# Kernel optimization log

Measured on AMD Instinct MI355X. Metric: run time of the kernel, lower is better.

## Reference

```python
import jax, jax.numpy as jnp
import numpy as np

B, N, D, H, E, W, OUT = 4, 2048, 128, 4, 32768, 8, 128


def setup_inputs() -> dict:
    key = jax.random.key(0)
    ks = jax.random.split(key, 11)
    s = 0.05  # weight init scale
    return {
        "nodefeatures": jax.random.normal(ks[0], (B, N, D), jnp.float32),
        "node_indices": jax.random.randint(ks[1], (B, 2, E), 0, N),
        "nodeattributes": jax.random.uniform(ks[2], (B, E, W), jnp.float32),
        "wq_w": jax.random.normal(ks[3], (H, D, D), jnp.float32) * s,
        "wq_b": jax.random.normal(ks[4], (H, D), jnp.float32) * s,
        "wk_w": jax.random.normal(ks[5], (H, D, D), jnp.float32) * s,
        "wk_b": jax.random.normal(ks[6], (H, D), jnp.float32) * s,
        "wv_w": jax.random.normal(ks[7], (H, D, D), jnp.float32) * s,
        "wv_b": jax.random.normal(ks[8], (H, D), jnp.float32) * s,
        "out_w": jax.random.normal(ks[9], (OUT, H * D), jnp.float32) * s,
        "out_b": jax.random.normal(ks[10], (OUT,), jnp.float32) * s,
    }


def reference(nodefeatures, node_indices, nodeattributes,
              wq_w, wq_b, wk_w, wk_b, wv_w, wv_b, out_w, out_b):
    b, n, d = nodefeatures.shape
    h = wq_w.shape[0]
    # per-head Linear projections: y = x @ W.T + bias, batched over heads -> [b,h,n,d]
    q = jnp.einsum('bnd,hed->bhne', nodefeatures, wq_w) + wq_b[None, :, None, :]
    k = jnp.einsum('bnd,hed->bhne', nodefeatures, wk_w) + wk_b[None, :, None, :]
    v = jnp.einsum('bnd,hed->bhne', nodefeatures, wv_w) + wv_b[None, :, None, :]

    i = node_indices[:, 0, :]  # [b,E] row indices
    j = node_indices[:, 1, :]  # [b,E] col indices

    # gather q_i, k_j per edge -> [b,h,E,d]; edge score = <q_i,k_j>/sqrt(n)
    qi = jnp.take_along_axis(q, i[:, None, :, None], axis=2)
    kj = jnp.take_along_axis(k, j[:, None, :, None], axis=2)
    wsum = nodeattributes.sum(axis=-1)  # [b,E] (x_edge[:,None]*weights).sum(1)
    # original divides by k.shape[1]**0.5 == sqrt(n)
    edge = (qi * kj).sum(-1) / (n ** 0.5) * wsum[:, None, :]  # [b,h,E]

    # scatter edge scores into zero-initialized dense logits [b,h,n,n]
    bi = jnp.arange(b)[:, None, None]
    hi = jnp.arange(h)[None, :, None]
    scores = jnp.zeros((b, h, n, n), q.dtype).at[bi, hi, i[:, None, :], j[:, None, :]].set(edge)

    attn = jax.nn.softmax(scores, axis=-1)
    o = jnp.einsum('bhnm,bhmd->bhnd', attn, v)
    o = o.transpose(0, 2, 1, 3).reshape(b, n, h * d)  # concat heads on feature dim
    return o @ out_w.T + out_b
```

## Files before the change

### kernel.cpp

```cpp
#include <hip/hip_runtime.h>
#include <hip/hip_bf16.h>
#include <math.h>

constexpr int B_ = 4;
constexpr int N_ = 2048;
constexpr int D_ = 128;
constexpr int H_ = 4;
constexpr int E_ = 32768;
constexpr int W_ = 8;
constexpr int OUT_ = 128;
constexpr int HD_ = H_ * D_;
constexpr int C3_ = 3 * HD_;
constexpr int CAP = 64;
constexpr int M_ = B_ * N_;

typedef __attribute__((ext_vector_type(8))) __bf16 bf16x8;
typedef __attribute__((ext_vector_type(4))) float f32x4;
typedef unsigned int uint32;
typedef unsigned short u16;

__device__ __forceinline__ u16 f2b(float f) {
    __hip_bfloat16 h = __float2bfloat16(f);
    return *(u16*)&h;
}
__device__ __forceinline__ float blo(uint32 u) { return __uint_as_float(u << 16); }
__device__ __forceinline__ float bhi(uint32 u) { return __uint_as_float(u & 0xffff0000u); }

__device__ __forceinline__ void g2l16(const void* g, void* l) {
    __builtin_amdgcn_global_load_lds(
        (const __attribute__((address_space(1))) unsigned int*)(uintptr_t)g,
        (__attribute__((address_space(3))) unsigned int*)(uintptr_t)l,
        16, 0, 0);
}

__global__ __launch_bounds__(256) void prep_kernel(
    const float* __restrict__ X,
    const float* __restrict__ wq, const float* __restrict__ wk, const float* __restrict__ wv,
    const float* __restrict__ bq, const float* __restrict__ bk, const float* __restrict__ bv,
    const float* __restrict__ OW,
    u16* __restrict__ Xbf, u16* __restrict__ Wbf, float* __restrict__ biasf,
    u16* __restrict__ OWbf,
    int* __restrict__ row_count, float* __restrict__ vsum)
{
    const int blk = blockIdx.x;
    if (blk < 512) {
        const int tid = blk * 256 + threadIdx.x;
        const int row = tid >> 4, sub = tid & 15;
        const float4 f0 = *(const float4*)(X + (size_t)row * 128 + sub * 8);
        const float4 f1 = *(const float4*)(X + (size_t)row * 128 + sub * 8 + 4);
        union { u16 u[8]; uint4 v; } pk;
        pk.u[0]=f2b(f0.x); pk.u[1]=f2b(f0.y); pk.u[2]=f2b(f0.z); pk.u[3]=f2b(f0.w);
        pk.u[4]=f2b(f1.x); pk.u[5]=f2b(f1.y); pk.u[6]=f2b(f1.z); pk.u[7]=f2b(f1.w);
        const int ob = row * 256 + ((sub * 16) ^ ((row & 7) << 4));
        *(uint4*)((char*)Xbf + ob) = pk.v;
    } else if (blk < 608) {
        const int c = (blk - 512) * 256 + threadIdx.x;
        const int g = c >> 11, idx = c & 2047;
        const int t3 = g >> 2, h = g & 3;
        const float* Wsrc = (t3 == 0 ? wq : t3 == 1 ? wk : wv) + (size_t)h * 128 * 128;
        const int e = idx >> 4, sub = idx & 15;
        const float4 f0 = *(const float4*)(Wsrc + (size_t)e * 128 + sub * 8);
        const float4 f1 = *(const float4*)(Wsrc + (size_t)e * 128 + sub * 8 + 4);
        union { u16 u[8]; uint4 v; } pk;
        pk.u[0]=f2b(f0.x); pk.u[1]=f2b(f0.y); pk.u[2]=f2b(f0.z); pk.u[3]=f2b(f0.w);
        pk.u[4]=f2b(f1.x); pk.u[5]=f2b(f1.y); pk.u[6]=f2b(f1.z); pk.u[7]=f2b(f1.w);
        const int ob = g * 32768 + e * 256 + ((sub * 16) ^ ((e & 7) << 4));
        *(uint4*)((char*)Wbf + ob) = pk.v;
        if (idx < 128) {
            const float* Bsrc = (t3 == 0 ? bq : t3 == 1 ? bk : bv) + h * 128;
            biasf[g * 128 + idx] = Bsrc[idx];
        }
    } else if (blk < 640) {
        const int tid = (blk - 608) * 256 + threadIdx.x;
        const int c = tid >> 6, sub = tid & 63;
        const float4 f0 = *(const float4*)(OW + (size_t)c * 512 + sub * 8);
        const float4 f1 = *(const float4*)(OW + (size_t)c * 512 + sub * 8 + 4);
        union { u16 u[8]; uint4 v; } pk;
        pk.u[0]=f2b(f0.x); pk.u[1]=f2b(f0.y); pk.u[2]=f2b(f0.z); pk.u[3]=f2b(f0.w);
        pk.u[4]=f2b(f1.x); pk.u[5]=f2b(f1.y); pk.u[6]=f2b(f1.z); pk.u[7]=f2b(f1.w);
        const int ob = c * 1024 + ((sub * 16) ^ ((c & 7) << 4));
        *(uint4*)((char*)OWbf + ob) = pk.v;
    } else {
        const uint4 z = make_uint4(0, 0, 0, 0);
        uint4* rc = (uint4*)row_count;
        #pragma unroll
        for (int q = 0; q < 8; ++q) rc[threadIdx.x + q * 256] = z;
        uint4* vs = (uint4*)vsum;
        #pragma unroll
        for (int q = 0; q < 2; ++q) vs[threadIdx.x + q * 256] = z;
    }
}

__global__ __launch_bounds__(256) void append_kernel(
    const int* __restrict__ nidx, const float* __restrict__ attr,
    int* __restrict__ row_count, int2* __restrict__ row_edges)
{
    const int wave = threadIdx.x >> 6;
    const int lane = threadIdx.x & 63;
    const int gw = blockIdx.x * 4 + wave;
    const int e0g = gw * 8;
    const int b = e0g / E_;
    const int e0 = e0g % E_;

    float a = attr[((size_t)b * E_ + e0) * W_ + lane];
    a += __shfl_xor(a, 1);
    a += __shfl_xor(a, 2);
    a += __shfl_xor(a, 4);

    if ((lane & 7) == 0) {
        const int sub = lane >> 3;
        const int e = e0 + sub;
        const int i = nidx[b * 2 * E_ + e];
        const int j = nidx[b * 2 * E_ + E_ + e];
        const int pos = atomicAdd(&row_count[b * N_ + i], 1);
        if (pos < CAP)
            row_edges[(size_t)(b * N_ + i) * CAP + pos] =
                make_int2(e | (j << 16), __float_as_int(a));
    }
}

__global__ __launch_bounds__(256) void qkv_mfma(
    const u16* __restrict__ Xbf, const u16* __restrict__ Wbf,
    const float* __restrict__ biasf, u16* __restrict__ QKV,
    float* __restrict__ vsum)
{
    __shared__ u16 As[128 * 128];
    __shared__ u16 Bs[128 * 128];
    const int rb = blockIdx.x & 63;
    const int g  = blockIdx.x >> 6;
    const int t = threadIdx.x;
    const int lane = t & 63, wave = t >> 6;
    const int wm = wave >> 1, wn = wave & 1;
    const int l15 = lane & 15, l4 = lane >> 4;

    const char* Asrc = (const char*)(Xbf + (size_t)rb * 128 * 128);
    const char* Bsrc = (const char*)(Wbf + (size_t)g  * 128 * 128);
    #pragma unroll
    for (int q = 0; q < 8; ++q) {
        const int o = t * 16 + q * 4096;
        g2l16(Asrc + o, (char*)As + o);
        g2l16(Bsrc + o, (char*)Bs + o);
    }
    __syncthreads();

    f32x4 acc[4][4];
    #pragma unroll
    for (int i = 0; i < 4; ++i)
        #pragma unroll
        for (int j = 0; j < 4; ++j) acc[i][j] = (f32x4){0.f, 0.f, 0.f, 0.f};

    #pragma unroll
    for (int ks = 0; ks < 4; ++ks) {
        const int kb = ks * 64 + l4 * 16;
        bf16x8 a[4], bb[4];
        #pragma unroll
        for (int fm = 0; fm < 4; ++fm) {
            const int row = wm * 64 + fm * 16 + l15;
            a[fm] = *(const bf16x8*)((const char*)As + row * 256 + (kb ^ ((row & 7) << 4)));
        }
        #pragma unroll
        for (int fn = 0; fn < 4; ++fn) {
            const int col = wn * 64 + fn * 16 + l15;
            bb[fn] = *(const bf16x8*)((const char*)Bs + col * 256 + (kb ^ ((col & 7) << 4)));
        }
        #pragma unroll
        for (int fm = 0; fm < 4; ++fm)
            #pragma unroll
            for (int fn = 0; fn < 4; ++fn)
                acc[fm][fn] = __builtin_amdgcn_mfma_f32_16x16x32_bf16(
                    a[fm], bb[fn], acc[fm][fn], 0, 0, 0);
    }

    __syncthreads();

    #pragma unroll
    for (int fm = 0; fm < 4; ++fm)
        #pragma unroll
        for (int fn = 0; fn < 4; ++fn) {
            const int col = wn * 64 + fn * 16 + l15;
            const float bv = biasf[g * 128 + col];
            #pragma unroll
            for (int r = 0; r < 4; ++r) {
                const int row = wm * 64 + fm * 16 + l4 * 4 + r;
                *(u16*)((char*)As + row * 256 + ((col * 2) ^ ((row & 7) << 4))) =
                    f2b(acc[fm][fn][r] + bv);
            }
        }

    if (g >= 8) {
        const int h = g - 8;
        const int b = rb >> 4;
        #pragma unroll
        for (int fn = 0; fn < 4; ++fn) {
            float s = 0.f;
            #pragma unroll
            for (int fm = 0; fm < 4; ++fm)
                #pragma unroll
                for (int r = 0; r < 4; ++r) s += acc[fm][fn][r];
            s += __shfl_xor(s, 16);
            s += __shfl_xor(s, 32);
            if (l4 == 0) {
                const int col = wn * 64 + fn * 16 + l15;
                const float bv = biasf[g * 128 + col];
                atomicAdd(&vsum[(b * H_ + h) * 128 + col], s + 64.f * bv);
            }
        }
    }
    __syncthreads();

    #pragma unroll
    for (int q = 0; q < 8; ++q) {
        const int idx = t + q * 256;
        const int row = idx >> 4, c = idx & 15;
        const uint4 v = *(const uint4*)((char*)As + row * 256 + ((c * 16) ^ ((row & 7) << 4)));
        *(uint4*)(QKV + (size_t)(rb * 128 + row) * C3_ + g * 128 + c * 8) = v;
    }
}

__global__ __launch_bounds__(256) void row_fused(
    const u16* __restrict__ QKV, const float* __restrict__ vsum,
    const int* __restrict__ row_count, const int2* __restrict__ row_edges,
    u16* __restrict__ Obf)
{
    const int t = threadIdx.x;
    const int wave = t >> 6, lane = t & 63;
    const int row = blockIdx.x * 4 + wave;
    const int b = blockIdx.y;
    const int R = b * N_ + row;
    int cnt = row_count[R];
    if (cnt > CAP) cnt = CAP;

    int ej = 0; float ws = 0.f;
    if (lane < cnt) {
        const int2 v = row_edges[(size_t)R * CAP + lane];
        ej = v.x; ws = __int_as_float(v.y);
    }
    const int myj = ej >> 16, mye = ej & 0xFFFF;
    bool win = (lane < cnt);
    for (int p = 0; p < cnt; ++p) {
        const int oj = __shfl(ej, p);
        if (win && (oj >> 16) == myj && (oj & 0xFFFF) > mye) win = false;
    }
    unsigned long long m = __ballot(win);

    const char* base = (const char*)QKV;
    const uint4 qv = *(const uint4*)(base + (size_t)R * 3072 + lane * 16);
    const float q0=blo(qv.x), q1=bhi(qv.x), q2=blo(qv.y), q3=bhi(qv.y),
                q4=blo(qv.z), q5=bhi(qv.z), q6=blo(qv.w), q7=bhi(qv.w);
    const float rs = 0.02209708691207961f;

    float a0=0.f,a1=0.f,a2=0.f,a3=0.f,a4=0.f,a5=0.f,a6=0.f,a7=0.f;
    float dsum = 0.f;

#define PROCESS(kv, vv, wsp)                                                  \
    {                                                                         \
        float s = q0*blo(kv.x) + q1*bhi(kv.x) + q2*blo(kv.y) + q3*bhi(kv.y)   \
                + q4*blo(kv.z) + q5*bhi(kv.z) + q6*blo(kv.w) + q7*bhi(kv.w);  \
        s += __shfl_xor(s, 1);                                                \
        s += __shfl_xor(s, 2);                                                \
        s += __shfl_xor(s, 4);                                                \
        s += __shfl_xor(s, 8);                                                \
        const float x = expf(s * rs * (wsp)) - 1.f;                           \
        dsum += x;                                                            \
        a0 = fmaf(x, blo(vv.x), a0); a1 = fmaf(x, bhi(vv.x), a1);             \
        a2 = fmaf(x, blo(vv.y), a2); a3 = fmaf(x, bhi(vv.y), a3);             \
        a4 = fmaf(x, blo(vv.z), a4); a5 = fmaf(x, bhi(vv.z), a5);             \
        a6 = fmaf(x, blo(vv.w), a6); a7 = fmaf(x, bhi(vv.w), a7);             \
    }

    if (m) {
        int p = (int)__ffsll(m) - 1; m &= m - 1;
        int jc = __shfl(ej, p) >> 16;
        float wc = __shfl(ws, p);
        const char* nb = base + (size_t)(b * N_ + jc) * 3072;
        uint4 kv = *(const uint4*)(nb + 1024 + lane * 16);
        uint4 vv = *(const uint4*)(nb + 2048 + lane * 16);
        while (m) {
            const int p2 = (int)__ffsll(m) - 1; m &= m - 1;
            const int j2 = __shfl(ej, p2) >> 16;
            const float w2 = __shfl(ws, p2);
            const char* nb2 = base + (size_t)(b * N_ + j2) * 3072;
            const uint4 kv2 = *(const uint4*)(nb2 + 1024 + lane * 16);
            const uint4 vv2 = *(const uint4*)(nb2 + 2048 + lane * 16);
            PROCESS(kv, vv, wc);
            kv = kv2; vv = vv2; wc = w2;
        }
        PROCESS(kv, vv, wc);
    }
#undef PROCESS

    const float inv = 1.0f / (2048.0f + dsum);
    const float* vsp = vsum + (b * H_ + (lane >> 4)) * 128 + (lane & 15) * 8;
    const float4 vs0 = *(const float4*)vsp;
    const float4 vs1 = *(const float4*)(vsp + 4);
    union { u16 u[8]; uint4 v; } o;
    o.u[0]=f2b((vs0.x+a0)*inv); o.u[1]=f2b((vs0.y+a1)*inv);
    o.u[2]=f2b((vs0.z+a2)*inv); o.u[3]=f2b((vs0.w+a3)*inv);
    o.u[4]=f2b((vs1.x+a4)*inv); o.u[5]=f2b((vs1.y+a5)*inv);
    o.u[6]=f2b((vs1.z+a6)*inv); o.u[7]=f2b((vs1.w+a7)*inv);
    const int ob = ((lane >> 4) << 8) + (((lane & 15) * 16) ^ ((R & 7) << 4));
    *(uint4*)((char*)Obf + (size_t)R * 1024 + ob) = o.v;
}

__global__ __launch_bounds__(256) void out_mfma(
    const u16* __restrict__ Obf, const u16* __restrict__ OWbf,
    const float* __restrict__ bo, float* __restrict__ Out)
{
    __shared__ u16 As[64 * 128];
    __shared__ u16 Bs[128 * 128];
    const int rb = blockIdx.x;
    const int t = threadIdx.x;
    const int lane = t & 63, wave = t >> 6;
    const int wm = wave >> 1, wn = wave & 1;
    const int l15 = lane & 15, l4 = lane >> 4;

    f32x4 acc[2][4];
    #pragma unroll
    for (int i = 0; i < 2; ++i)
        #pragma unroll
        for (int j = 0; j < 4; ++j) acc[i][j] = (f32x4){0.f, 0.f, 0.f, 0.f};

    for (int kc = 0; kc < 4; ++kc) {
        #pragma unroll
        for (int q = 0; q < 4; ++q) {
            const int o = t * 16 + q * 4096;
            const int arow = o >> 8, ob = o & 255;
            g2l16((const char*)Obf + (size_t)(rb * 64 + arow) * 1024 + kc * 256 + ob,
                  (char*)As + o);
        }
        #pragma unroll
        for (int q = 0; q < 8; ++q) {
            const int o = t * 16 + q * 4096;
            const int c = o >> 8, ob = o & 255;
            g2l16((const char*)OWbf + (size_t)c * 1024 + kc * 256 + ob,
                  (char*)Bs + o);
        }
        __syncthreads();
        #pragma unroll
        for (int ks = 0; ks < 4; ++ks) {
            const int kb = ks * 64 + l4 * 16;
            bf16x8 a[2], bb[4];
            #pragma unroll
            for (int fm = 0; fm < 2; ++fm) {
                const int row = wm * 32 + fm * 16 + l15;
                a[fm] = *(const bf16x8*)((const char*)As + row * 256 + (kb ^ ((row & 7) << 4)));
            }
            #pragma unroll
            for (int fn = 0; fn < 4; ++fn) {
                const int col = wn * 64 + fn * 16 + l15;
                bb[fn] = *(const bf16x8*)((const char*)Bs + col * 256 + (kb ^ ((col & 7) << 4)));
            }
            #pragma unroll
            for (int fm = 0; fm < 2; ++fm)
                #pragma unroll
                for (int fn = 0; fn < 4; ++fn)
                    acc[fm][fn] = __builtin_amdgcn_mfma_f32_16x16x32_bf16(
                        a[fm], bb[fn], acc[fm][fn], 0, 0, 0);
        }
        __syncthreads();
    }

    #pragma unroll
    for (int fm = 0; fm < 2; ++fm)
        #pragma unroll
        for (int fn = 0; fn < 4; ++fn) {
            const int col = wn * 64 + fn * 16 + l15;
            const float bv = bo[col];
            #pragma unroll
            for (int r = 0; r < 4; ++r) {
                const int row = rb * 64 + wm * 32 + fm * 16 + l4 * 4 + r;
                Out[(size_t)row * OUT_ + col] = acc[fm][fn][r] + bv;
            }
        }
}

extern "C" void kernel_launch(void* const* d_in, const int* in_sizes, int n_in,
                              void* d_out, int out_size, void* d_ws, size_t ws_size,
                              hipStream_t stream)
{
    const float* x     = (const float*)d_in[0];
    const int*   nidx  = (const int*)  d_in[1];
    const float* attr  = (const float*)d_in[2];
    const float* wq_w  = (const float*)d_in[3];
    const float* wq_b  = (const float*)d_in[4];
    const float* wk_w  = (const float*)d_in[5];
    const float* wk_b  = (const float*)d_in[6];
    const float* wv_w  = (const float*)d_in[7];
    const float* wv_b  = (const float*)d_in[8];
    const float* out_w = (const float*)d_in[9];
    const float* out_b = (const float*)d_in[10];
    float* out = (float*)d_out;

    char* ws = (char*)d_ws;
    size_t off = 0;
    auto alloc = [&](size_t bytes) -> char* {
        char* p = ws + off;
        off += (bytes + 255) & ~(size_t)255;
        return p;
    };
    u16*  Xbf  = (u16*)alloc((size_t)M_ * D_ * 2);
    u16*  Wbf  = (u16*)alloc((size_t)12 * D_ * D_ * 2);
    float* biasf = (float*)alloc((size_t)12 * D_ * 4);
    u16*  QKV  = (u16*)alloc((size_t)M_ * C3_ * 2);
    u16*  OWbf = (u16*)alloc((size_t)OUT_ * HD_ * 2);
    u16*  Obf  = (u16*)alloc((size_t)M_ * HD_ * 2);
    float* vsum = (float*)alloc((size_t)B_ * H_ * D_ * 4);
    int*  row_count = (int*)alloc((size_t)B_ * N_ * 4);
    int2* row_edges = (int2*)alloc((size_t)B_ * N_ * CAP * 8);

    prep_kernel<<<641, 256, 0, stream>>>(
        x, wq_w, wk_w, wv_w, wq_b, wk_b, wv_b, out_w,
        Xbf, Wbf, biasf, OWbf, row_count, vsum);
    append_kernel<<<(B_ * E_) / 32, 256, 0, stream>>>(nidx, attr, row_count, row_edges);
    qkv_mfma<<<64 * 12, 256, 0, stream>>>(Xbf, Wbf, biasf, QKV, vsum);
    row_fused<<<dim3(N_ / 4, B_), 256, 0, stream>>>(
        QKV, vsum, row_count, row_edges, Obf);
    out_mfma<<<M_ / 64, 256, 0, stream>>>(Obf, OWbf, out_b, out);
}
```

Measured before the change: 84.24 us.

## Fuse edge append into QKV GEMM launch, double-buffer gathers, shrink output tiles

The edge-append pass now runs inside the QKV GEMM launch: 256 extra blocks, each looping 16 times, do the append alongside the 768 GEMM blocks. This removes one kernel launch and lets the append overlap the GEMM. The row kernel now fetches two neighbour K/V rows per step into two accumulator sets, which gives more memory-level parallelism. The output GEMM uses 32-row tiles, doubling the block count for better occupancy at the cost of reloading the weight tile more often. The appended blocks still allocate the GEMM's large shared memory, and the extra registers in the row kernel may lower its occupancy.

Result: faster. 79.18 us (-6.0%).

```diff
diff --git a/kernel.cpp b/kernel.cpp
--- a/kernel.cpp
+++ b/kernel.cpp
@@ -91,45 +91,45 @@
     }
 }
 
-__global__ __launch_bounds__(256) void append_kernel(
+__global__ __launch_bounds__(256) void qkv_append(
+    const u16* __restrict__ Xbf, const u16* __restrict__ Wbf,
+    const float* __restrict__ biasf,
     const int* __restrict__ nidx, const float* __restrict__ attr,
+    u16* __restrict__ QKV, float* __restrict__ vsum,
     int* __restrict__ row_count, int2* __restrict__ row_edges)
-{
-    const int wave = threadIdx.x >> 6;
-    const int lane = threadIdx.x & 63;
-    const int gw = blockIdx.x * 4 + wave;
-    const int e0g = gw * 8;
-    const int b = e0g / E_;
-    const int e0 = e0g % E_;
-
-    float a = attr[((size_t)b * E_ + e0) * W_ + lane];
-    a += __shfl_xor(a, 1);
-    a += __shfl_xor(a, 2);
-    a += __shfl_xor(a, 4);
-
-    if ((lane & 7) == 0) {
-        const int sub = lane >> 3;
-        const int e = e0 + sub;
-        const int i = nidx[b * 2 * E_ + e];
-        const int j = nidx[b * 2 * E_ + E_ + e];
-        const int pos = atomicAdd(&row_count[b * N_ + i], 1);
-        if (pos < CAP)
-            row_edges[(size_t)(b * N_ + i) * CAP + pos] =
-                make_int2(e | (j << 16), __float_as_int(a));
-    }
-}
-
-__global__ __launch_bounds__(256) void qkv_mfma(
-    const u16* __restrict__ Xbf, const u16* __restrict__ Wbf,
-    const float* __restrict__ biasf, u16* __restrict__ QKV,
-    float* __restrict__ vsum)
 {
     __shared__ u16 As[128 * 128];
     __shared__ u16 Bs[128 * 128];
+    const int t = threadIdx.x;
+    const int lane = t & 63, wave = t >> 6;
+
+    if (blockIdx.x >= 768) {
+        const int gw0 = (blockIdx.x - 768) * 4 + wave;
+        for (int it = 0; it < 16; ++it) {
+            const int gw = gw0 + it * 1024;
+            const int e0g = gw * 8;
+            const int b = e0g / E_;
+            const int e0 = e0g % E_;
+            float a = attr[((size_t)b * E_ + e0) * W_ + lane];
+            a += __shfl_xor(a, 1);
+            a += __shfl_xor(a, 2);
+            a += __shfl_xor(a, 4);
+            if ((lane & 7) == 0) {
+                const int sub = lane >> 3;
+                const int e = e0 + sub;
+                const int i = nidx[b * 2 * E_ + e];
+                const int j = nidx[b * 2 * E_ + E_ + e];
+                const int pos = atomicAdd(&row_count[b * N_ + i], 1);
+                if (pos < CAP)
+                    row_edges[(size_t)(b * N_ + i) * CAP + pos] =
+                        make_int2(e | (j << 16), __float_as_int(a));
+            }
+        }
+        return;
+    }
+
     const int rb = blockIdx.x & 63;
     const int g  = blockIdx.x >> 6;
-    const int t = threadIdx.x;
-    const int lane = t & 63, wave = t >> 6;
     const int wm = wave >> 1, wn = wave & 1;
     const int l15 = lane & 15, l4 = lane >> 4;
 
@@ -249,55 +249,65 @@
                 q4=blo(qv.z), q5=bhi(qv.z), q6=blo(qv.w), q7=bhi(qv.w);
     const float rs = 0.02209708691207961f;
 
-    float a0=0.f,a1=0.f,a2=0.f,a3=0.f,a4=0.f,a5=0.f,a6=0.f,a7=0.f;
-    float dsum = 0.f;
-
-#define PROCESS(kv, vv, wsp)                                                  \
-    {                                                                         \
-        float s = q0*blo(kv.x) + q1*bhi(kv.x) + q2*blo(kv.y) + q3*bhi(kv.y)   \
-                + q4*blo(kv.z) + q5*bhi(kv.z) + q6*blo(kv.w) + q7*bhi(kv.w);  \
-        s += __shfl_xor(s, 1);                                                \
-        s += __shfl_xor(s, 2);                                                \
-        s += __shfl_xor(s, 4);                                                \
-        s += __shfl_xor(s, 8);                                                \
-        const float x = expf(s * rs * (wsp)) - 1.f;                           \
-        dsum += x;                                                            \
-        a0 = fmaf(x, blo(vv.x), a0); a1 = fmaf(x, bhi(vv.x), a1);             \
-        a2 = fmaf(x, blo(vv.y), a2); a3 = fmaf(x, bhi(vv.y), a3);             \
-        a4 = fmaf(x, blo(vv.z), a4); a5 = fmaf(x, bhi(vv.z), a5);             \
-        a6 = fmaf(x, blo(vv.w), a6); a7 = fmaf(x, bhi(vv.w), a7);             \
-    }
+    float A0=0.f,A1=0.f,A2=0.f,A3=0.f,A4=0.f,A5=0.f,A6=0.f,A7=0.f;
+    float B0=0.f,B1=0.f,B2=0.f,B3=0.f,B4=0.f,B5=0.f,B6=0.f,B7=0.f;
+    float dsA = 0.f, dsB = 0.f;
+
+#define FETCH(MM, KV1,VV1,W1,KV2,VV2,W2,NN)                                  \
+    { int p_ = (int)__ffsll((long long)MM) - 1; MM &= MM - 1;                \
+      const int j_ = __shfl(ej, p_) >> 16; W1 = __shfl(ws, p_);              \
+      const char* nb_ = base + (size_t)(b * N_ + j_) * 3072;                 \
+      KV1 = *(const uint4*)(nb_ + 1024 + lane * 16);                         \
+      VV1 = *(const uint4*)(nb_ + 2048 + lane * 16);                         \
+      if (MM) {                                                              \
+        int q_ = (int)__ffsll((long long)MM) - 1; MM &= MM - 1;              \
+        const int j2_ = __shfl(ej, q_) >> 16; W2 = __shfl(ws, q_);           \
+        const char* nb2_ = base + (size_t)(b * N_ + j2_) * 3072;             \
+        KV2 = *(const uint4*)(nb2_ + 1024 + lane * 16);                      \
+        VV2 = *(const uint4*)(nb2_ + 2048 + lane * 16);                      \
+        NN = 2;                                                              \
+      } else NN = 1; }
+
+#define PROC(kv, vv, wsp, S)                                                 \
+    { float s_ = q0*blo(kv.x) + q1*bhi(kv.x) + q2*blo(kv.y) + q3*bhi(kv.y)   \
+               + q4*blo(kv.z) + q5*bhi(kv.z) + q6*blo(kv.w) + q7*bhi(kv.w);  \
+      s_ += __shfl_xor(s_, 1);                                               \
+      s_ += __shfl_xor(s_, 2);                                               \
+      s_ += __shfl_xor(s_, 4);                                               \
+      s_ += __shfl_xor(s_, 8);                                               \
+      const float x_ = expf(s_ * rs * (wsp)) - 1.f;                          \
+      ds##S += x_;                                                           \
+      S##0 = fmaf(x_, blo(vv.x), S##0); S##1 = fmaf(x_, bhi(vv.x), S##1);    \
+      S##2 = fmaf(x_, blo(vv.y), S##2); S##3 = fmaf(x_, bhi(vv.y), S##3);    \
+      S##4 = fmaf(x_, blo(vv.z), S##4); S##5 = fmaf(x_, bhi(vv.z), S##5);    \
+      S##6 = fmaf(x_, blo(vv.w), S##6); S##7 = fmaf(x_, bhi(vv.w), S##7); }
 
     if (m) {
-        int p = (int)__ffsll(m) - 1; m &= m - 1;
-        int jc = __shfl(ej, p) >> 16;
-        float wc = __shfl(ws, p);
-        const char* nb = base + (size_t)(b * N_ + jc) * 3072;
-        uint4 kv = *(const uint4*)(nb + 1024 + lane * 16);
-        uint4 vv = *(const uint4*)(nb + 2048 + lane * 16);
+        uint4 kv1, vv1, kv2, vv2; float w1, w2; int n1;
+        FETCH(m, kv1, vv1, w1, kv2, vv2, w2, n1);
         while (m) {
-            const int p2 = (int)__ffsll(m) - 1; m &= m - 1;
-            const int j2 = __shfl(ej, p2) >> 16;
-            const float w2 = __shfl(ws, p2);
-            const char* nb2 = base + (size_t)(b * N_ + j2) * 3072;
-            const uint4 kv2 = *(const uint4*)(nb2 + 1024 + lane * 16);
-            const uint4 vv2 = *(const uint4*)(nb2 + 2048 + lane * 16);
-            PROCESS(kv, vv, wc);
-            kv = kv2; vv = vv2; wc = w2;
-        }
-        PROCESS(kv, vv, wc);
-    }
-#undef PROCESS
-
-    const float inv = 1.0f / (2048.0f + dsum);
+            uint4 nk1, nv1, nk2, nv2; float nw1, nw2; int n2;
+            FETCH(m, nk1, nv1, nw1, nk2, nv2, nw2, n2);
+            PROC(kv1, vv1, w1, A);
+            if (n1 == 2) PROC(kv2, vv2, w2, B);
+            kv1 = nk1; vv1 = nv1; w1 = nw1;
+            kv2 = nk2; vv2 = nv2; w2 = nw2; n1 = n2;
+        }
+        PROC(kv1, vv1, w1, A);
+        if (n1 == 2) PROC(kv2, vv2, w2, B);
+    }
+#undef FETCH
+#undef PROC
+
+    const float inv = 1.0f / (2048.0f + dsA + dsB);
     const float* vsp = vsum + (b * H_ + (lane >> 4)) * 128 + (lane & 15) * 8;
     const float4 vs0 = *(const float4*)vsp;
     const float4 vs1 = *(const float4*)(vsp + 4);
     union { u16 u[8]; uint4 v; } o;
-    o.u[0]=f2b((vs0.x+a0)*inv); o.u[1]=f2b((vs0.y+a1)*inv);
-    o.u[2]=f2b((vs0.z+a2)*inv); o.u[3]=f2b((vs0.w+a3)*inv);
-    o.u[4]=f2b((vs1.x+a4)*inv); o.u[5]=f2b((vs1.y+a5)*inv);
-    o.u[6]=f2b((vs1.z+a6)*inv); o.u[7]=f2b((vs1.w+a7)*inv);
+    o.u[0]=f2b((vs0.x+A0+B0)*inv); o.u[1]=f2b((vs0.y+A1+B1)*inv);
+    o.u[2]=f2b((vs0.z+A2+B2)*inv); o.u[3]=f2b((vs0.w+A3+B3)*inv);
+    o.u[4]=f2b((vs1.x+A4+B4)*inv); o.u[5]=f2b((vs1.y+A5+B5)*inv);
+    o.u[6]=f2b((vs1.z+A6+B6)*inv); o.u[7]=f2b((vs1.w+A7+B7)*inv);
     const int ob = ((lane >> 4) << 8) + (((lane & 15) * 16) ^ ((R & 7) << 4));
     *(uint4*)((char*)Obf + (size_t)R * 1024 + ob) = o.v;
 }
@@ -306,7 +316,7 @@
     const u16* __restrict__ Obf, const u16* __restrict__ OWbf,
     const float* __restrict__ bo, float* __restrict__ Out)
 {
-    __shared__ u16 As[64 * 128];
+    __shared__ u16 As[32 * 128];
     __shared__ u16 Bs[128 * 128];
     const int rb = blockIdx.x;
     const int t = threadIdx.x;
@@ -314,18 +324,16 @@
     const int wm = wave >> 1, wn = wave & 1;
     const int l15 = lane & 15, l4 = lane >> 4;
 
-    f32x4 acc[2][4];
-    #pragma unroll
-    for (int i = 0; i < 2; ++i)
-        #pragma unroll
-        for (int j = 0; j < 4; ++j) acc[i][j] = (f32x4){0.f, 0.f, 0.f, 0.f};
+    f32x4 acc[4];
+    #pragma unroll
+    for (int j = 0; j < 4; ++j) acc[j] = (f32x4){0.f, 0.f, 0.f, 0.f};
 
     for (int kc = 0; kc < 4; ++kc) {
         #pragma unroll
-        for (int q = 0; q < 4; ++q) {
+        for (int q = 0; q < 2; ++q) {
             const int o = t * 16 + q * 4096;
             const int arow = o >> 8, ob = o & 255;
-            g2l16((const char*)Obf + (size_t)(rb * 64 + arow) * 1024 + kc * 256 + ob,
+            g2l16((const char*)Obf + (size_t)(rb * 32 + arow) * 1024 + kc * 256 + ob,
                   (char*)As + o);
         }
         #pragma unroll
@@ -339,11 +347,10 @@
         #pragma unroll
         for (int ks = 0; ks < 4; ++ks) {
             const int kb = ks * 64 + l4 * 16;
-            bf16x8 a[2], bb[4];
-            #pragma unroll
-            for (int fm = 0; fm < 2; ++fm) {
-                const int row = wm * 32 + fm * 16 + l15;
-                a[fm] = *(const bf16x8*)((const char*)As + row * 256 + (kb ^ ((row & 7) << 4)));
+            bf16x8 a0, bb[4];
+            {
+                const int row = wm * 16 + l15;
+                a0 = *(const bf16x8*)((const char*)As + row * 256 + (kb ^ ((row & 7) << 4)));
             }
             #pragma unroll
             for (int fn = 0; fn < 4; ++fn) {
@@ -351,27 +358,23 @@
                 bb[fn] = *(const bf16x8*)((const char*)Bs + col * 256 + (kb ^ ((col & 7) << 4)));
             }
             #pragma unroll
-            for (int fm = 0; fm < 2; ++fm)
-                #pragma unroll
-                for (int fn = 0; fn < 4; ++fn)
-                    acc[fm][fn] = __builtin_amdgcn_mfma_f32_16x16x32_bf16(
-                        a[fm], bb[fn], acc[fm][fn], 0, 0, 0);
+            for (int fn = 0; fn < 4; ++fn)
+                acc[fn] = __builtin_amdgcn_mfma_f32_16x16x32_bf16(
+                    a0, bb[fn], acc[fn], 0, 0, 0);
         }
         __syncthreads();
     }
 
     #pragma unroll
-    for (int fm = 0; fm < 2; ++fm)
-        #pragma unroll
-        for (int fn = 0; fn < 4; ++fn) {
-            const int col = wn * 64 + fn * 16 + l15;
-            const float bv = bo[col];
-            #pragma unroll
-            for (int r = 0; r < 4; ++r) {
-                const int row = rb * 64 + wm * 32 + fm * 16 + l4 * 4 + r;
-                Out[(size_t)row * OUT_ + col] = acc[fm][fn][r] + bv;
-            }
-        }
+    for (int fn = 0; fn < 4; ++fn) {
+        const int col = wn * 64 + fn * 16 + l15;
+        const float bv = bo[col];
+        #pragma unroll
+        for (int r = 0; r < 4; ++r) {
+            const int row = rb * 32 + wm * 16 + l4 * 4 + r;
+            Out[(size_t)row * OUT_ + col] = acc[fn][r] + bv;
+        }
+    }
 }
 
 extern "C" void kernel_launch(void* const* d_in, const int* in_sizes, int n_in,
@@ -411,9 +414,9 @@
     prep_kernel<<<641, 256, 0, stream>>>(
         x, wq_w, wk_w, wv_w, wq_b, wk_b, wv_b, out_w,
         Xbf, Wbf, biasf, OWbf, row_count, vsum);
-    append_kernel<<<(B_ * E_) / 32, 256, 0, stream>>>(nidx, attr, row_count, row_edges);
-    qkv_mfma<<<64 * 12, 256, 0, stream>>>(Xbf, Wbf, biasf, QKV, vsum);
+    qkv_append<<<1024, 256, 0, stream>>>(
+        Xbf, Wbf, biasf, nidx, attr, QKV, vsum, row_count, row_edges);
     row_fused<<<dim3(N_ / 4, B_), 256, 0, stream>>>(
         QKV, vsum, row_count, row_edges, Obf);
-    out_mfma<<<M_ / 64, 256, 0, stream>>>(Obf, OWbf, out_b, out);
-}
+    out_mfma<<<M_ / 32, 256, 0, stream>>>(Obf, OWbf, out_b, out);
+}
```
